# Kernel tuning notes

Hardware: AMD Instinct MI355X
Metric: run time of the kernel (lower is better)

## Reference

```python
import jax, jax.numpy as jnp
import numpy as np

IN_C, OUT_C, HEADS = 128, 64, 2
N_USER, N_ITEM, E = 100000, 50000, 500000
NEG_SLOPE = 0.2


def _params(key, in_c, out_c, heads):
    ks = jax.random.split(key, 4)
    s_lin = 1.0 / np.sqrt(in_c)
    s_att = 1.0 / np.sqrt(out_c)
    return dict(
        Wl=jax.random.normal(ks[0], (in_c, heads * out_c), jnp.float32) * s_lin,
        bl=jnp.zeros((heads * out_c,), jnp.float32),
        Wr=jax.random.normal(ks[1], (in_c, heads * out_c), jnp.float32) * s_lin,
        br=jnp.zeros((heads * out_c,), jnp.float32),
        att=jax.random.normal(ks[2], (heads, out_c), jnp.float32) * s_att,
        bias=jnp.zeros((out_c,), jnp.float32),
    )


def setup_inputs() -> dict:
    key = jax.random.key(0)
    k = jax.random.split(key, 8)
    inp = {
        "x_user": jax.random.normal(k[0], (N_USER, IN_C), jnp.float32),
        "x_item": jax.random.normal(k[1], (N_ITEM, IN_C), jnp.float32),
        "src_u2i": jax.random.randint(k[2], (E,), 0, N_USER, jnp.int32),
        "dst_u2i": jax.random.randint(k[3], (E,), 0, N_ITEM, jnp.int32),
        "src_i2u": jax.random.randint(k[4], (E,), 0, N_ITEM, jnp.int32),
        "dst_i2u": jax.random.randint(k[5], (E,), 0, N_USER, jnp.int32),
    }
    p_u2i = _params(k[6], IN_C, OUT_C, HEADS)
    p_i2u = _params(k[7], IN_C, OUT_C, HEADS)
    for n, v in p_u2i.items():
        inp[n + "_u2i"] = v
    for n, v in p_i2u.items():
        inp[n + "_i2u"] = v
    return inp


def gatv2_conv(x_src, x_dst, src, dst, Wl, bl, Wr, br, att, bias, n_dst):
    # lin_l on source nodes, lin_r on destination nodes -> [N, H, C]
    xl = (x_src @ Wl + bl).reshape(-1, HEADS, OUT_C)
    xr = (x_dst @ Wr + br).reshape(-1, HEADS, OUT_C)
    xj = xl[src]  # [E, H, C] gathered source features
    xi = xr[dst]  # [E, H, C] gathered dest features
    e = jax.nn.leaky_relu(xi + xj, NEG_SLOPE)
    logits = jnp.einsum("ehc,hc->eh", e, att)  # [E, H]
    # numerically stable segment softmax over incoming edges per dest node
    m = jax.ops.segment_max(logits, dst, num_segments=n_dst)
    m = jnp.where(jnp.isfinite(m), m, 0.0)  # guard empty segments
    a = jnp.exp(logits - m[dst])
    denom = jax.ops.segment_sum(a, dst, num_segments=n_dst)
    alpha = a / (denom[dst] + 1e-16)
    out = jax.ops.segment_sum(alpha[:, :, None] * xj, dst, num_segments=n_dst)
    return out.mean(axis=1) + bias  # concat=False -> head mean, then bias


def reference(x_user, x_item, src_u2i, dst_u2i, src_i2u, dst_i2u,
              Wl_u2i, bl_u2i, Wr_u2i, br_u2i, att_u2i, bias_u2i,
              Wl_i2u, bl_i2u, Wr_i2u, br_i2u, att_i2u, bias_i2u):
    # HeteroConv with aggr='sum': one edge type per destination node type here
    out_item = gatv2_conv(x_user, x_item, src_u2i, dst_u2i,
                          Wl_u2i, bl_u2i, Wr_u2i, br_u2i, att_u2i, bias_u2i, N_ITEM)
    out_user = gatv2_conv(x_item, x_user, src_i2u, dst_i2u,
                          Wl_i2u, bl_i2u, Wr_i2u, br_i2u, att_i2u, bias_i2u, N_USER)
    return out_user, out_item
```

## Files before the change

kernel.cpp:

```cpp
#include <hip/hip_runtime.h>

#define SCAN_B 1024

__global__ __launch_bounds__(256) void k_zero(int* __restrict__ cnt, int n) {
    int i = blockIdx.x * 256 + threadIdx.x;
    if (i < n) cnt[i] = 0;
}

__global__ __launch_bounds__(256) void k_hist(
    const int* __restrict__ dst_a, const int* __restrict__ dst_b,
    int* __restrict__ cnt, int n_a, int E)
{
    int i = blockIdx.x * 256 + threadIdx.x;
    if (i >= 2 * E) return;
    int idx = (i < E) ? dst_a[i] : (n_a + dst_b[i - E]);
    atomicAdd(&cnt[idx], 1);
}

__global__ __launch_bounds__(SCAN_B) void k_scan1(
    const int* __restrict__ cnt, int n, int* __restrict__ rowptr, int* __restrict__ bsum)
{
    __shared__ int tmp[SCAN_B];
    int i = blockIdx.x * SCAN_B + threadIdx.x;
    int v = (i < n) ? cnt[i] : 0;
    tmp[threadIdx.x] = v;
    __syncthreads();
    for (int off = 1; off < SCAN_B; off <<= 1) {
        int t = (threadIdx.x >= (unsigned)off) ? tmp[threadIdx.x - off] : 0;
        __syncthreads();
        tmp[threadIdx.x] += t;
        __syncthreads();
    }
    if (i < n) rowptr[i] = tmp[threadIdx.x] - v;
    if (threadIdx.x == SCAN_B - 1) bsum[blockIdx.x] = tmp[threadIdx.x];
}

__global__ __launch_bounds__(SCAN_B) void k_scan2(int* __restrict__ bsum, int nb) {
    __shared__ int tmp[SCAN_B];
    int i = threadIdx.x;
    int v = (i < nb) ? bsum[i] : 0;
    tmp[i] = v;
    __syncthreads();
    for (int off = 1; off < SCAN_B; off <<= 1) {
        int t = (i >= off) ? tmp[i - off] : 0;
        __syncthreads();
        tmp[i] += t;
        __syncthreads();
    }
    if (i < nb) bsum[i] = tmp[i] - v;
}

__global__ __launch_bounds__(256) void k_scan3(
    int* __restrict__ rowptr, int* __restrict__ cursor,
    const int* __restrict__ bsum, int n, int total)
{
    int i = blockIdx.x * 256 + threadIdx.x;
    if (i < n) {
        int r = rowptr[i] + bsum[i / SCAN_B];
        rowptr[i] = r;
        cursor[i] = r;
    }
    if (i == 0) rowptr[n] = total;
}

__global__ __launch_bounds__(256) void k_fill(
    const int* __restrict__ src_a, const int* __restrict__ dst_a,
    const int* __restrict__ src_b, const int* __restrict__ dst_b,
    int* __restrict__ cursor, int* __restrict__ sorted_src, int n_a, int E)
{
    int i = blockIdx.x * 256 + threadIdx.x;
    if (i >= 2 * E) return;
    int idx, s;
    if (i < E) { idx = dst_a[i];            s = src_a[i]; }
    else       { idx = n_a + dst_b[i - E];  s = src_b[i - E]; }
    int pos = atomicAdd(&cursor[idx], 1);
    sorted_src[pos] = s;
}

__global__ __launch_bounds__(256) void gemm128(
    const float* __restrict__ X, const float* __restrict__ W,
    const float* __restrict__ Bv, float* __restrict__ Y, int M)
{
    __shared__ float xs[64][36];
    __shared__ float ws[32][128];

    const int tid = threadIdx.x;
    const int m0  = blockIdx.x * 64;
    const int r0  = (tid >> 4) * 4;
    const int c0  = (tid & 15) * 4;

    float acc[4][8];
#pragma unroll
    for (int i = 0; i < 4; ++i)
#pragma unroll
        for (int j = 0; j < 8; ++j) acc[i][j] = 0.0f;

    for (int kc = 0; kc < 128; kc += 32) {
#pragma unroll
        for (int i = 0; i < 2; ++i) {
            int f = tid + i * 256;
            int row = f >> 3;
            int kq  = (f & 7) * 4;
            float4 v = make_float4(0.f, 0.f, 0.f, 0.f);
            if (m0 + row < M)
                v = *(const float4*)&X[(size_t)(m0 + row) * 128 + kc + kq];
            *(float4*)&xs[row][kq] = v;
        }
#pragma unroll
        for (int i = 0; i < 4; ++i) {
            int f = tid + i * 256;
            int k  = f >> 5;
            int nq = (f & 31) * 4;
            *(float4*)&ws[k][nq] = *(const float4*)&W[(size_t)(kc + k) * 128 + nq];
        }
        __syncthreads();

#pragma unroll
        for (int k = 0; k < 32; k += 4) {
            float4 a0 = *(const float4*)&xs[r0 + 0][k];
            float4 a1 = *(const float4*)&xs[r0 + 1][k];
            float4 a2 = *(const float4*)&xs[r0 + 2][k];
            float4 a3 = *(const float4*)&xs[r0 + 3][k];
#pragma unroll
            for (int kk = 0; kk < 4; ++kk) {
                float4 b0 = *(const float4*)&ws[k + kk][c0];
                float4 b1 = *(const float4*)&ws[k + kk][c0 + 64];
                float bx0 = b0.x, bx1 = b0.y, bx2 = b0.z, bx3 = b0.w;
                float bx4 = b1.x, bx5 = b1.y, bx6 = b1.z, bx7 = b1.w;
                float av0 = ((const float*)&a0)[kk];
                float av1 = ((const float*)&a1)[kk];
                float av2 = ((const float*)&a2)[kk];
                float av3 = ((const float*)&a3)[kk];
                acc[0][0] += av0 * bx0; acc[0][1] += av0 * bx1;
                acc[0][2] += av0 * bx2; acc[0][3] += av0 * bx3;
                acc[0][4] += av0 * bx4; acc[0][5] += av0 * bx5;
                acc[0][6] += av0 * bx6; acc[0][7] += av0 * bx7;
                acc[1][0] += av1 * bx0; acc[1][1] += av1 * bx1;
                acc[1][2] += av1 * bx2; acc[1][3] += av1 * bx3;
                acc[1][4] += av1 * bx4; acc[1][5] += av1 * bx5;
                acc[1][6] += av1 * bx6; acc[1][7] += av1 * bx7;
                acc[2][0] += av2 * bx0; acc[2][1] += av2 * bx1;
                acc[2][2] += av2 * bx2; acc[2][3] += av2 * bx3;
                acc[2][4] += av2 * bx4; acc[2][5] += av2 * bx5;
                acc[2][6] += av2 * bx6; acc[2][7] += av2 * bx7;
                acc[3][0] += av3 * bx0; acc[3][1] += av3 * bx1;
                acc[3][2] += av3 * bx2; acc[3][3] += av3 * bx3;
                acc[3][4] += av3 * bx4; acc[3][5] += av3 * bx5;
                acc[3][6] += av3 * bx6; acc[3][7] += av3 * bx7;
            }
        }
        __syncthreads();
    }

    float4 bb0 = *(const float4*)&Bv[c0];
    float4 bb1 = *(const float4*)&Bv[c0 + 64];
#pragma unroll
    for (int i = 0; i < 4; ++i) {
        int row = m0 + r0 + i;
        if (row < M) {
            float4 o0 = make_float4(acc[i][0] + bb0.x, acc[i][1] + bb0.y,
                                    acc[i][2] + bb0.z, acc[i][3] + bb0.w);
            float4 o1 = make_float4(acc[i][4] + bb1.x, acc[i][5] + bb1.y,
                                    acc[i][6] + bb1.z, acc[i][7] + bb1.w);
            *(float4*)&Y[(size_t)row * 128 + c0]      = o0;
            *(float4*)&Y[(size_t)row * 128 + c0 + 64] = o1;
        }
    }
}

__global__ __launch_bounds__(256) void k_gat(
    const float* __restrict__ xl, const float* __restrict__ xr,
    const float* __restrict__ att, const float* __restrict__ bias,
    const int* __restrict__ rowptr, const int* __restrict__ srcs,
    float* __restrict__ out, int n_dst)
{
    int wave = (blockIdx.x * 256 + threadIdx.x) >> 6;
    if (wave >= n_dst) return;
    const int lane = threadIdx.x & 63;
    const int h = lane >> 5;
    const int j = lane & 31;
    const int c0 = h * 64 + j;
    const int c1 = c0 + 32;
    const int d = wave;

    const int base = rowptr[d];
    const int end  = rowptr[d + 1];
    if (base == end) {
        if (lane < 32) {
            out[(size_t)d * 64 + j]      = bias[j];
            out[(size_t)d * 64 + j + 32] = bias[j + 32];
        }
        return;
    }

    const float xi0 = xr[(size_t)d * 128 + c0];
    const float xi1 = xr[(size_t)d * 128 + c1];
    const float at0 = att[c0];
    const float at1 = att[c1];

    float m = -3.4e38f, den = 0.f, a0 = 0.f, a1 = 0.f;
    int s = srcs[base];
    for (int k = base; k < end; ++k) {
        int sc = s;
        if (k + 1 < end) s = srcs[k + 1];
        const float* xjp = xl + (size_t)sc * 128;
        float xj0 = xjp[c0];
        float xj1 = xjp[c1];
        float e0 = xi0 + xj0;
        float e1 = xi1 + xj1;
        e0 = e0 >= 0.f ? e0 : 0.2f * e0;
        e1 = e1 >= 0.f ? e1 : 0.2f * e1;
        float p = e0 * at0 + e1 * at1;
        p += __shfl_xor(p, 1, 64);
        p += __shfl_xor(p, 2, 64);
        p += __shfl_xor(p, 4, 64);
        p += __shfl_xor(p, 8, 64);
        p += __shfl_xor(p, 16, 64);
        float mn  = fmaxf(m, p);
        float scl = __expf(m - mn);
        float w   = __expf(p - mn);
        a0  = a0 * scl + w * xj0;
        a1  = a1 * scl + w * xj1;
        den = den * scl + w;
        m = mn;
    }

    float inv = 1.0f / (den + 1e-16f);
    float r0 = a0 * inv;
    float r1 = a1 * inv;
    float q0 = __shfl_xor(r0, 32, 64);
    float q1 = __shfl_xor(r1, 32, 64);
    if (lane < 32) {
        out[(size_t)d * 64 + j]      = 0.5f * (r0 + q0) + bias[j];
        out[(size_t)d * 64 + j + 32] = 0.5f * (r1 + q1) + bias[j + 32];
    }
}

extern "C" void kernel_launch(void* const* d_in, const int* in_sizes, int n_in,
                              void* d_out, int out_size, void* d_ws, size_t ws_size,
                              hipStream_t stream)
{
    const float* x_user   = (const float*)d_in[0];
    const float* x_item   = (const float*)d_in[1];
    const int*   src_u2i  = (const int*)d_in[2];
    const int*   dst_u2i  = (const int*)d_in[3];
    const int*   src_i2u  = (const int*)d_in[4];
    const int*   dst_i2u  = (const int*)d_in[5];
    const float* Wl_u2i   = (const float*)d_in[6];
    const float* bl_u2i   = (const float*)d_in[7];
    const float* Wr_u2i   = (const float*)d_in[8];
    const float* br_u2i   = (const float*)d_in[9];
    const float* att_u2i  = (const float*)d_in[10];
    const float* bias_u2i = (const float*)d_in[11];
    const float* Wl_i2u   = (const float*)d_in[12];
    const float* bl_i2u   = (const float*)d_in[13];
    const float* Wr_i2u   = (const float*)d_in[14];
    const float* br_i2u   = (const float*)d_in[15];
    const float* att_i2u  = (const float*)d_in[16];
    const float* bias_i2u = (const float*)d_in[17];

    const int n_user = in_sizes[0] / 128;
    const int n_item = in_sizes[1] / 128;
    const int E      = in_sizes[2];
    const int n_all  = n_item + n_user;

    float* out_user = (float*)d_out;
    float* out_item = out_user + (size_t)n_user * 64;

    char* w = (char*)d_ws;
    float* xl_u2i = (float*)w; w += (size_t)n_user * 128 * 4;
    float* xr_u2i = (float*)w; w += (size_t)n_item * 128 * 4;
    float* xl_i2u = (float*)w; w += (size_t)n_item * 128 * 4;
    float* xr_i2u = (float*)w; w += (size_t)n_user * 128 * 4;
    int* srcs_all   = (int*)w; w += (size_t)2 * E * 4;
    int* rowptr_all = (int*)w; w += (size_t)(n_all + 1) * 4;
    int* cnt_all    = (int*)w; w += (size_t)n_all * 4;
    int* bsum       = (int*)w; w += (size_t)SCAN_B * 4;

    const int nb = (n_all + SCAN_B - 1) / SCAN_B;

    k_zero<<<(n_all + 255) / 256, 256, 0, stream>>>(cnt_all, n_all);
    k_hist<<<(2 * E + 255) / 256, 256, 0, stream>>>(dst_u2i, dst_i2u, cnt_all, n_item, E);
    k_scan1<<<nb, SCAN_B, 0, stream>>>(cnt_all, n_all, rowptr_all, bsum);
    k_scan2<<<1, SCAN_B, 0, stream>>>(bsum, nb);
    k_scan3<<<(n_all + 255) / 256, 256, 0, stream>>>(rowptr_all, cnt_all, bsum, n_all, 2 * E);
    k_fill<<<(2 * E + 255) / 256, 256, 0, stream>>>(
        src_u2i, dst_u2i, src_i2u, dst_i2u, cnt_all, srcs_all, n_item, E);

    gemm128<<<(n_user + 63) / 64, 256, 0, stream>>>(x_user, Wl_u2i, bl_u2i, xl_u2i, n_user);
    gemm128<<<(n_item + 63) / 64, 256, 0, stream>>>(x_item, Wr_u2i, br_u2i, xr_u2i, n_item);
    gemm128<<<(n_item + 63) / 64, 256, 0, stream>>>(x_item, Wl_i2u, bl_i2u, xl_i2u, n_item);
    gemm128<<<(n_user + 63) / 64, 256, 0, stream>>>(x_user, Wr_i2u, br_i2u, xr_i2u, n_user);

    k_gat<<<(n_item + 3) / 4, 256, 0, stream>>>(
        xl_u2i, xr_u2i, att_u2i, bias_u2i, rowptr_all, srcs_all, out_item, n_item);
    k_gat<<<(n_user + 3) / 4, 256, 0, stream>>>(
        xl_i2u, xr_i2u, att_i2u, bias_i2u, rowptr_all + n_item, srcs_all, out_user, n_user);
}
```

Baseline: 507.6 us.

## Fuse paired GEMMs sharing input, merge GAT launches, unroll edge loop by two

Pairs the two linear projections that read the same node features into one kernel computing 256 output columns, so each input matrix is read once. The two per-edge-type attention kernels become one launch indexed over all destination nodes. The online softmax loop processes two edges per iteration, putting more independent gathers in flight. In exchange, the GEMM holds more accumulators per thread, which raises register pressure.

```diff
diff --git a/kernel.cpp b/kernel.cpp
--- a/kernel.cpp
+++ b/kernel.cpp
@@ -77,23 +77,25 @@
     sorted_src[pos] = s;
 }
 
-__global__ __launch_bounds__(256) void gemm128(
-    const float* __restrict__ X, const float* __restrict__ W,
-    const float* __restrict__ Bv, float* __restrict__ Y, int M)
+__global__ __launch_bounds__(256) void gemm128x2(
+    const float* __restrict__ X,
+    const float* __restrict__ W0, const float* __restrict__ B0, float* __restrict__ Y0,
+    const float* __restrict__ W1, const float* __restrict__ B1, float* __restrict__ Y1,
+    int M)
 {
     __shared__ float xs[64][36];
-    __shared__ float ws[32][128];
+    __shared__ float ws[32][256];
 
     const int tid = threadIdx.x;
     const int m0  = blockIdx.x * 64;
     const int r0  = (tid >> 4) * 4;
     const int c0  = (tid & 15) * 4;
 
-    float acc[4][8];
+    float acc[4][16];
 #pragma unroll
     for (int i = 0; i < 4; ++i)
 #pragma unroll
-        for (int j = 0; j < 8; ++j) acc[i][j] = 0.0f;
+        for (int j = 0; j < 16; ++j) acc[i][j] = 0.0f;
 
     for (int kc = 0; kc < 128; kc += 32) {
 #pragma unroll
@@ -107,11 +109,14 @@
             *(float4*)&xs[row][kq] = v;
         }
 #pragma unroll
-        for (int i = 0; i < 4; ++i) {
+        for (int i = 0; i < 8; ++i) {
             int f = tid + i * 256;
-            int k  = f >> 5;
-            int nq = (f & 31) * 4;
-            *(float4*)&ws[k][nq] = *(const float4*)&W[(size_t)(kc + k) * 128 + nq];
+            int k = f >> 6;
+            int q = (f & 63) * 4;
+            float4 v = (q < 128)
+                ? *(const float4*)&W0[(size_t)(kc + k) * 128 + q]
+                : *(const float4*)&W1[(size_t)(kc + k) * 128 + (q - 128)];
+            *(float4*)&ws[k][q] = v;
         }
         __syncthreads();
 
@@ -125,66 +130,73 @@
             for (int kk = 0; kk < 4; ++kk) {
                 float4 b0 = *(const float4*)&ws[k + kk][c0];
                 float4 b1 = *(const float4*)&ws[k + kk][c0 + 64];
-                float bx0 = b0.x, bx1 = b0.y, bx2 = b0.z, bx3 = b0.w;
-                float bx4 = b1.x, bx5 = b1.y, bx6 = b1.z, bx7 = b1.w;
-                float av0 = ((const float*)&a0)[kk];
-                float av1 = ((const float*)&a1)[kk];
-                float av2 = ((const float*)&a2)[kk];
-                float av3 = ((const float*)&a3)[kk];
-                acc[0][0] += av0 * bx0; acc[0][1] += av0 * bx1;
-                acc[0][2] += av0 * bx2; acc[0][3] += av0 * bx3;
-                acc[0][4] += av0 * bx4; acc[0][5] += av0 * bx5;
-                acc[0][6] += av0 * bx6; acc[0][7] += av0 * bx7;
-                acc[1][0] += av1 * bx0; acc[1][1] += av1 * bx1;
-                acc[1][2] += av1 * bx2; acc[1][3] += av1 * bx3;
-                acc[1][4] += av1 * bx4; acc[1][5] += av1 * bx5;
-                acc[1][6] += av1 * bx6; acc[1][7] += av1 * bx7;
-                acc[2][0] += av2 * bx0; acc[2][1] += av2 * bx1;
-                acc[2][2] += av2 * bx2; acc[2][3] += av2 * bx3;
-                acc[2][4] += av2 * bx4; acc[2][5] += av2 * bx5;
-                acc[2][6] += av2 * bx6; acc[2][7] += av2 * bx7;
-                acc[3][0] += av3 * bx0; acc[3][1] += av3 * bx1;
-                acc[3][2] += av3 * bx2; acc[3][3] += av3 * bx3;
-                acc[3][4] += av3 * bx4; acc[3][5] += av3 * bx5;
-                acc[3][6] += av3 * bx6; acc[3][7] += av3 * bx7;
+                float4 b2 = *(const float4*)&ws[k + kk][c0 + 128];
+                float4 b3 = *(const float4*)&ws[k + kk][c0 + 192];
+                float av[4] = { ((const float*)&a0)[kk], ((const float*)&a1)[kk],
+                                ((const float*)&a2)[kk], ((const float*)&a3)[kk] };
+#pragma unroll
+                for (int i = 0; i < 4; ++i) {
+                    float a = av[i];
+                    acc[i][0]  += a * b0.x; acc[i][1]  += a * b0.y;
+                    acc[i][2]  += a * b0.z; acc[i][3]  += a * b0.w;
+                    acc[i][4]  += a * b1.x; acc[i][5]  += a * b1.y;
+                    acc[i][6]  += a * b1.z; acc[i][7]  += a * b1.w;
+                    acc[i][8]  += a * b2.x; acc[i][9]  += a * b2.y;
+                    acc[i][10] += a * b2.z; acc[i][11] += a * b2.w;
+                    acc[i][12] += a * b3.x; acc[i][13] += a * b3.y;
+                    acc[i][14] += a * b3.z; acc[i][15] += a * b3.w;
+                }
             }
         }
         __syncthreads();
     }
 
-    float4 bb0 = *(const float4*)&Bv[c0];
-    float4 bb1 = *(const float4*)&Bv[c0 + 64];
+    float4 p00 = *(const float4*)&B0[c0];
+    float4 p01 = *(const float4*)&B0[c0 + 64];
+    float4 p10 = *(const float4*)&B1[c0];
+    float4 p11 = *(const float4*)&B1[c0 + 64];
 #pragma unroll
     for (int i = 0; i < 4; ++i) {
         int row = m0 + r0 + i;
         if (row < M) {
-            float4 o0 = make_float4(acc[i][0] + bb0.x, acc[i][1] + bb0.y,
-                                    acc[i][2] + bb0.z, acc[i][3] + bb0.w);
-            float4 o1 = make_float4(acc[i][4] + bb1.x, acc[i][5] + bb1.y,
-                                    acc[i][6] + bb1.z, acc[i][7] + bb1.w);
-            *(float4*)&Y[(size_t)row * 128 + c0]      = o0;
-            *(float4*)&Y[(size_t)row * 128 + c0 + 64] = o1;
-        }
-    }
-}
-
-__global__ __launch_bounds__(256) void k_gat(
-    const float* __restrict__ xl, const float* __restrict__ xr,
-    const float* __restrict__ att, const float* __restrict__ bias,
+            *(float4*)&Y0[(size_t)row * 128 + c0] = make_float4(
+                acc[i][0] + p00.x, acc[i][1] + p00.y, acc[i][2] + p00.z, acc[i][3] + p00.w);
+            *(float4*)&Y0[(size_t)row * 128 + c0 + 64] = make_float4(
+                acc[i][4] + p01.x, acc[i][5] + p01.y, acc[i][6] + p01.z, acc[i][7] + p01.w);
+            *(float4*)&Y1[(size_t)row * 128 + c0] = make_float4(
+                acc[i][8] + p10.x, acc[i][9] + p10.y, acc[i][10] + p10.z, acc[i][11] + p10.w);
+            *(float4*)&Y1[(size_t)row * 128 + c0 + 64] = make_float4(
+                acc[i][12] + p11.x, acc[i][13] + p11.y, acc[i][14] + p11.z, acc[i][15] + p11.w);
+        }
+    }
+}
+
+__global__ __launch_bounds__(256) void k_gat2(
+    const float* __restrict__ xl_a, const float* __restrict__ xr_a,
+    const float* __restrict__ att_a, const float* __restrict__ bias_a,
+    float* __restrict__ out_a,
+    const float* __restrict__ xl_b, const float* __restrict__ xr_b,
+    const float* __restrict__ att_b, const float* __restrict__ bias_b,
+    float* __restrict__ out_b,
     const int* __restrict__ rowptr, const int* __restrict__ srcs,
-    float* __restrict__ out, int n_dst)
+    int n_a, int n_all)
 {
     int wave = (blockIdx.x * 256 + threadIdx.x) >> 6;
-    if (wave >= n_dst) return;
+    if (wave >= n_all) return;
     const int lane = threadIdx.x & 63;
     const int h = lane >> 5;
     const int j = lane & 31;
     const int c0 = h * 64 + j;
     const int c1 = c0 + 32;
-    const int d = wave;
-
-    const int base = rowptr[d];
-    const int end  = rowptr[d + 1];
+
+    const float *xl, *xr, *att, *bias;
+    float* out;
+    int d;
+    if (wave < n_a) { xl = xl_a; xr = xr_a; att = att_a; bias = bias_a; out = out_a; d = wave; }
+    else            { xl = xl_b; xr = xr_b; att = att_b; bias = bias_b; out = out_b; d = wave - n_a; }
+
+    const int base = rowptr[wave];
+    const int end  = rowptr[wave + 1];
     if (base == end) {
         if (lane < 32) {
             out[(size_t)d * 64 + j]      = bias[j];
@@ -199,29 +211,55 @@
     const float at1 = att[c1];
 
     float m = -3.4e38f, den = 0.f, a0 = 0.f, a1 = 0.f;
-    int s = srcs[base];
-    for (int k = base; k < end; ++k) {
-        int sc = s;
-        if (k + 1 < end) s = srcs[k + 1];
-        const float* xjp = xl + (size_t)sc * 128;
-        float xj0 = xjp[c0];
-        float xj1 = xjp[c1];
-        float e0 = xi0 + xj0;
-        float e1 = xi1 + xj1;
-        e0 = e0 >= 0.f ? e0 : 0.2f * e0;
-        e1 = e1 >= 0.f ? e1 : 0.2f * e1;
-        float p = e0 * at0 + e1 * at1;
-        p += __shfl_xor(p, 1, 64);
-        p += __shfl_xor(p, 2, 64);
-        p += __shfl_xor(p, 4, 64);
-        p += __shfl_xor(p, 8, 64);
-        p += __shfl_xor(p, 16, 64);
-        float mn  = fmaxf(m, p);
+    int k = base;
+    for (; k + 1 < end; k += 2) {
+        int s0 = srcs[k];
+        int s1 = srcs[k + 1];
+        const float* xp0 = xl + (size_t)s0 * 128;
+        const float* xp1 = xl + (size_t)s1 * 128;
+        float x00 = xp0[c0], x01 = xp0[c1];
+        float x10 = xp1[c0], x11 = xp1[c1];
+        float e00 = xi0 + x00, e01 = xi1 + x01;
+        float e10 = xi0 + x10, e11 = xi1 + x11;
+        e00 = e00 >= 0.f ? e00 : 0.2f * e00;
+        e01 = e01 >= 0.f ? e01 : 0.2f * e01;
+        e10 = e10 >= 0.f ? e10 : 0.2f * e10;
+        e11 = e11 >= 0.f ? e11 : 0.2f * e11;
+        float p0 = e00 * at0 + e01 * at1;
+        float p1 = e10 * at0 + e11 * at1;
+        p0 += __shfl_xor(p0, 1, 64);  p1 += __shfl_xor(p1, 1, 64);
+        p0 += __shfl_xor(p0, 2, 64);  p1 += __shfl_xor(p1, 2, 64);
+        p0 += __shfl_xor(p0, 4, 64);  p1 += __shfl_xor(p1, 4, 64);
+        p0 += __shfl_xor(p0, 8, 64);  p1 += __shfl_xor(p1, 8, 64);
+        p0 += __shfl_xor(p0, 16, 64); p1 += __shfl_xor(p1, 16, 64);
+        float mn  = fmaxf(m, fmaxf(p0, p1));
         float scl = __expf(m - mn);
-        float w   = __expf(p - mn);
-        a0  = a0 * scl + w * xj0;
-        a1  = a1 * scl + w * xj1;
-        den = den * scl + w;
+        float w0  = __expf(p0 - mn);
+        float w1  = __expf(p1 - mn);
+        den = den * scl + w0 + w1;
+        a0  = a0 * scl + w0 * x00 + w1 * x10;
+        a1  = a1 * scl + w0 * x01 + w1 * x11;
+        m = mn;
+    }
+    if (k < end) {
+        int s0 = srcs[k];
+        const float* xp0 = xl + (size_t)s0 * 128;
+        float x00 = xp0[c0], x01 = xp0[c1];
+        float e00 = xi0 + x00, e01 = xi1 + x01;
+        e00 = e00 >= 0.f ? e00 : 0.2f * e00;
+        e01 = e01 >= 0.f ? e01 : 0.2f * e01;
+        float p0 = e00 * at0 + e01 * at1;
+        p0 += __shfl_xor(p0, 1, 64);
+        p0 += __shfl_xor(p0, 2, 64);
+        p0 += __shfl_xor(p0, 4, 64);
+        p0 += __shfl_xor(p0, 8, 64);
+        p0 += __shfl_xor(p0, 16, 64);
+        float mn  = fmaxf(m, p0);
+        float scl = __expf(m - mn);
+        float w0  = __expf(p0 - mn);
+        den = den * scl + w0;
+        a0  = a0 * scl + w0 * x00;
+        a1  = a1 * scl + w0 * x01;
         m = mn;
     }
 
@@ -287,13 +325,13 @@
     k_fill<<<(2 * E + 255) / 256, 256, 0, stream>>>(
         src_u2i, dst_u2i, src_i2u, dst_i2u, cnt_all, srcs_all, n_item, E);
 
-    gemm128<<<(n_user + 63) / 64, 256, 0, stream>>>(x_user, Wl_u2i, bl_u2i, xl_u2i, n_user);
-    gemm128<<<(n_item + 63) / 64, 256, 0, stream>>>(x_item, Wr_u2i, br_u2i, xr_u2i, n_item);
-    gemm128<<<(n_item + 63) / 64, 256, 0, stream>>>(x_item, Wl_i2u, bl_i2u, xl_i2u, n_item);
-    gemm128<<<(n_user + 63) / 64, 256, 0, stream>>>(x_user, Wr_i2u, br_i2u, xr_i2u, n_user);
-
-    k_gat<<<(n_item + 3) / 4, 256, 0, stream>>>(
-        xl_u2i, xr_u2i, att_u2i, bias_u2i, rowptr_all, srcs_all, out_item, n_item);
-    k_gat<<<(n_user + 3) / 4, 256, 0, stream>>>(
-        xl_i2u, xr_i2u, att_i2u, bias_i2u, rowptr_all + n_item, srcs_all, out_user, n_user);
-}
+    gemm128x2<<<(n_user + 63) / 64, 256, 0, stream>>>(
+        x_user, Wl_u2i, bl_u2i, xl_u2i, Wr_i2u, br_i2u, xr_i2u, n_user);
+    gemm128x2<<<(n_item + 63) / 64, 256, 0, stream>>>(
+        x_item, Wl_i2u, bl_i2u, xl_i2u, Wr_u2i, br_u2i, xr_u2i, n_item);
+
+    k_gat2<<<(n_all + 3) / 4, 256, 0, stream>>>(
+        xl_u2i, xr_u2i, att_u2i, bias_u2i, out_item,
+        xl_i2u, xr_i2u, att_i2u, bias_i2u, out_user,
+        rowptr_all, srcs_all, n_item, n_all);
+}
```

Result: faster. 478.5 us (-5.7%).
